# Optimization experiments

Hardware: AMD Instinct MI355X
Metric: run time of the kernel (lower is better)

Reference implementation:

```python
import jax, jax.numpy as jnp
import numpy as np

EPS_NORM = 1e-10
EPS_EXP = 1e-6


def setup_inputs() -> dict:
    key = jax.random.key(0)
    k1, k2 = jax.random.split(key)
    B, F, H, W = 16, 2048, 8, 8
    X = jax.random.normal(k1, (B, F, H, W), dtype=jnp.float32)
    M = jax.random.normal(k2, (B, F, H, W), dtype=jnp.float32)
    return {"X": X, "M": M}


def reference(X, M):
    B, F, H, W = X.shape
    N = H * W
    X = X.reshape(B, F, N)
    M = M.reshape(B, F, N)

    # feature centering over dim=-2 (the feature axis of (B, F, N))
    X = X - X.mean(axis=1, keepdims=True)
    M = M - M.mean(axis=1, keepdims=True)

    # feature_normalize: L2 norm over dim 1, keepdim, + eps
    X = X / (jnp.linalg.norm(X, axis=1, keepdims=True) + EPS_NORM)
    M = M / (jnp.linalg.norm(M, axis=1, keepdims=True) + EPS_NORM)

    # MatmulTopkLoss: S = X @ M^T over spatial N -> (B, F, F)
    S = jnp.einsum('bfn,bgn->bfg', X, M)
    YX = S + jnp.transpose(S, (0, 2, 1))  # symmetrize
    P = jax.nn.softmax(YX, axis=-1)

    k = F // 2
    value, idx = jax.lax.top_k(P, k)  # (B, F, k) values desc, indices
    value_sum = value.sum(axis=-1, keepdims=True)
    row_pos = jnp.arange(F)[None, :, None]  # (1, F, 1)
    dist = jnp.abs(idx - row_pos).astype(value.dtype)
    C_xy = (value * dist / value_sum).mean(axis=-1)  # (B, F)

    xy = jnp.exp(-C_xy + C_xy.min() - EPS_EXP)
    return jnp.reshape(xy.mean(), (1,))
```

## Files before the change

kernel.cpp:

```cpp
#include <hip/hip_runtime.h>
#include <hip/hip_bf16.h>
#include <math.h>

#define B_   16
#define F_   2048
#define N_   64
#define K_   1024
#define YP   2056

typedef short bf16x8 __attribute__((ext_vector_type(8)));
typedef float v4f    __attribute__((ext_vector_type(4)));

__device__ __forceinline__ float wave_sum(float v) {
#pragma unroll
  for (int off = 32; off > 0; off >>= 1) v += __shfl_down(v, off, 64);
  return v;
}
__device__ __forceinline__ float wave_max(float v) {
#pragma unroll
  for (int off = 32; off > 0; off >>= 1) v = fmaxf(v, __shfl_down(v, off, 64));
  return v;
}

__device__ __forceinline__ unsigned f2bf(float x) {
  const unsigned u = __float_as_uint(x);
  return (u + 0x7FFFu + ((u >> 16) & 1u)) >> 16;
}
__device__ __forceinline__ float bf2f(unsigned us) {
  return __uint_as_float(us << 16);
}
__device__ __forceinline__ unsigned ord2u16(unsigned T) {
  return (T & 0x8000u) ? (T ^ 0x8000u) : (T ^ 0xFFFFu);
}
__device__ __forceinline__ unsigned ordpair(unsigned wd) {
  return wd ^ (0x80008000u | (((wd & 0x80008000u) >> 15) * 0x7FFFu));
}

__global__ __launch_bounds__(256) void stats_kernel(
    const float* __restrict__ X, const float* __restrict__ M,
    float* __restrict__ P) {
  __shared__ float red[4][N_][4];
  const int tid = threadIdx.x;
  const int b = blockIdx.x >> 4;
  const int fb = blockIdx.x & 15;
  const int f0 = fb * 128;
  const int fi = tid >> 6, n = tid & 63;
  float sx = 0.f, sxx = 0.f, sm = 0.f, smm = 0.f;
#pragma unroll 4
  for (int j = 0; j < 32; ++j) {
    const int f = f0 + fi + 4 * j;
    const size_t gi = ((size_t)b * F_ + f) * N_ + n;
    const float x = X[gi];
    const float m = M[gi];
    sx += x; sxx += x * x; sm += m; smm += m * m;
  }
  red[fi][n][0] = sx; red[fi][n][1] = sxx;
  red[fi][n][2] = sm; red[fi][n][3] = smm;
  __syncthreads();
  const int wn = tid & 63, word = tid >> 6;
  const float s = red[0][wn][word] + red[1][wn][word] +
                  red[2][wn][word] + red[3][wn][word];
  P[(((size_t)b * N_ + wn) * 4 + word) * 16 + fb] = s;
}

__global__ __launch_bounds__(256) void normbf_kernel(
    const float* __restrict__ X, const float* __restrict__ M,
    const float* __restrict__ P,
    short* __restrict__ Xb16, short* __restrict__ Mb16) {
  const int tid = threadIdx.x;
  const int b = blockIdx.x >> 4;
  const int f0 = (blockIdx.x & 15) * 128;
  const int n = tid & 63;
  const float* base = P + (((size_t)b * N_ + n) * 4) * 16;
  float acc4[4];
#pragma unroll
  for (int wj = 0; wj < 4; ++wj) {
    float s = 0.f;
#pragma unroll
    for (int i = 0; i < 16; ++i) s += base[16 * wj + i];
    acc4[wj] = s;
  }
  const float sx = acc4[0], sxx = acc4[1], sm = acc4[2], smm = acc4[3];
  const float mux = sx * (1.f / F_), mum = sm * (1.f / F_);
  const float rx = 1.f / (sqrtf(fmaxf(sxx - (float)F_ * mux * mux, 0.f)) + 1e-10f);
  const float rm = 1.f / (sqrtf(fmaxf(smm - (float)F_ * mum * mum, 0.f)) + 1e-10f);
  const int s_ = n >> 5, q_ = (n >> 3) & 3, j_ = n & 7;
#pragma unroll 4
  for (int jj = 0; jj < 32; ++jj) {
    const int f = f0 + (tid >> 6) + 4 * jj;
    const size_t gi = ((size_t)b * F_ + f) * N_ + n;
    const int t16 = f >> 4, nl = f & 15;
    const size_t pi = (((size_t)b * 128 + t16) * 2 + s_) * 512 +
                      (q_ * 16 + nl) * 8 + j_;
    Xb16[pi] = (short)f2bf((X[gi] - mux) * rx);
    Mb16[pi] = (short)f2bf((M[gi] - mum) * rm);
  }
}

__global__ __launch_bounds__(512)
__attribute__((amdgpu_waves_per_eu(4, 4)))
void rows_kernel(
    const short* __restrict__ Xb16, const short* __restrict__ Mb16,
    float* __restrict__ C) {
  __shared__ unsigned short yxu[16 * YP];
  __shared__ unsigned histS[8 * 256];

  const int tid = threadIdx.x;
  const int w = tid >> 6, lane = tid & 63;
  const int nl = lane & 15, q = lane >> 4;
  const int b = blockIdx.x >> 7;
  const int f0 = (blockIdx.x & 127) * 16;
  const int g0 = 256 * w;

  const short* __restrict__ Xb = Xb16 + (size_t)b * F_ * N_;
  const short* __restrict__ Mb = Mb16 + (size_t)b * F_ * N_;

  const short* Axp = Xb + (size_t)(f0 >> 4) * 1024 + lane * 8;
  const short* Amp = Mb + (size_t)(f0 >> 4) * 1024 + lane * 8;
  const bf16x8 ax0 = *(const bf16x8*)(Axp);
  const bf16x8 ax1 = *(const bf16x8*)(Axp + 512);
  const bf16x8 am0 = *(const bf16x8*)(Amp);
  const bf16x8 am1 = *(const bf16x8*)(Amp + 512);

  v4f acc[16];
#pragma unroll
  for (int t = 0; t < 16; ++t) acc[t] = (v4f)(0.f);

#pragma unroll
  for (int t = 0; t < 16; ++t) {
    const short* Bmp = Mb + (size_t)(16 * w + t) * 1024 + lane * 8;
    const short* Bxp = Xb + (size_t)(16 * w + t) * 1024 + lane * 8;
    const bf16x8 bm0 = *(const bf16x8*)(Bmp);
    const bf16x8 bm1 = *(const bf16x8*)(Bmp + 512);
    const bf16x8 bx0 = *(const bf16x8*)(Bxp);
    const bf16x8 bx1 = *(const bf16x8*)(Bxp + 512);
    acc[t] = __builtin_amdgcn_mfma_f32_16x16x32_bf16(ax0, bm0, acc[t], 0, 0, 0);
    acc[t] = __builtin_amdgcn_mfma_f32_16x16x32_bf16(ax1, bm1, acc[t], 0, 0, 0);
    acc[t] = __builtin_amdgcn_mfma_f32_16x16x32_bf16(am0, bx0, acc[t], 0, 0, 0);
    acc[t] = __builtin_amdgcn_mfma_f32_16x16x32_bf16(am1, bx1, acc[t], 0, 0, 0);
  }

#pragma unroll
  for (int t = 0; t < 16; ++t) {
    const int col = g0 + 16 * t + nl;
#pragma unroll
    for (int r = 0; r < 4; ++r)
      yxu[(4 * q + r) * YP + col] = (unsigned short)f2bf(acc[t][r]);
  }
  __syncthreads();

  unsigned* wh = &histS[w << 8];
#pragma unroll 1
  for (int r4 = 0; r4 < 2; ++r4) {
    const int row = 2 * w + r4;
    const int frow = f0 + row;
    const uint4* rp = (const uint4*)(yxu + row * YP);

    unsigned pk[16];
    unsigned kmin = 0xFFFFFFFFu, kmax = 0u;
#pragma unroll
    for (int j = 0; j < 4; ++j) {
      const uint4 tt = rp[lane + 64 * j];
      const unsigned wds[4] = {tt.x, tt.y, tt.z, tt.w};
#pragma unroll
      for (int c = 0; c < 4; ++c) {
        const unsigned o = ordpair(wds[c]);
        pk[4 * j + c] = o;
        const unsigned o0 = o & 0xFFFFu, o1 = o >> 16;
        kmin = min(kmin, min(o0, o1));
        kmax = max(kmax, max(o0, o1));
      }
    }
#pragma unroll
    for (int off = 32; off > 0; off >>= 1) {
      kmin = min(kmin, (unsigned)__shfl_down((int)kmin, off, 64));
      kmax = max(kmax, (unsigned)__shfl_down((int)kmax, off, 64));
    }
    kmin = (unsigned)__shfl((int)kmin, 0, 64);
    kmax = (unsigned)__shfl((int)kmax, 0, 64);

    unsigned lo = kmin, R = kmax - kmin, krem = K_;
    unsigned T, tie_need;
    if (R == 0) {
      T = lo; tie_need = krem;
    } else {
      for (;;) {
        const int pos = 31 - __builtin_clz(R);
        const int sh = (pos > 7) ? (pos - 7) : 0;
#pragma unroll
        for (int i = 0; i < 4; ++i) wh[lane + 64 * i] = 0u;
        __builtin_amdgcn_wave_barrier();
#pragma unroll
        for (int c = 0; c < 16; ++c) {
          const unsigned o = pk[c];
          const unsigned d0 = (o & 0xFFFFu) - lo;
          const unsigned d1 = (o >> 16) - lo;
          if (d0 <= R) atomicAdd(&wh[d0 >> sh], 1u);
          if (d1 <= R) atomicAdd(&wh[d1 >> sh], 1u);
        }
        __builtin_amdgcn_wave_barrier();
        unsigned h[4];
#pragma unroll
        for (int i = 0; i < 4; ++i) h[i] = wh[4 * lane + i];
        unsigned s3 = h[3], s2 = h[2] + s3, s1 = h[1] + s2, s0 = h[0] + s1;
        unsigned tot = s0;
#pragma unroll
        for (int off = 1; off < 64; off <<= 1) {
          const unsigned v = __shfl_down(tot, off, 64);
          if (lane + off < 64) tot += v;
        }
        const unsigned above = tot - s0;
        const unsigned S[4] = {above + s0, above + s1, above + s2, above + s3};
        unsigned packed = 0;
        bool found = false;
#pragma unroll
        for (int i = 0; i < 4; ++i) {
          const unsigned Sip1 = S[i] - h[i];
          if (S[i] >= krem && Sip1 < krem) {
            packed = ((unsigned)(4 * lane + i) << 16) | Sip1;
            found = true;
          }
        }
        const unsigned long long bm = __ballot(found);
        const int winner = __ffsll(bm) - 1;
        packed = (unsigned)__shfl((int)packed, winner, 64);
        const unsigned D = packed >> 16;
        krem -= (packed & 0xFFFFu);
        if (sh == 0) { T = lo + D; tie_need = krem; break; }
        lo += (D << sh);
        R = (1u << sh) - 1u;
      }
    }

    float vs = 0.f, ws = 0.f;
    unsigned cnt[4];
#pragma unroll
    for (int j = 0; j < 4; ++j) {
      cnt[j] = 0;
#pragma unroll
      for (int c = 0; c < 4; ++c) {
        const unsigned o = pk[4 * j + c];
        const unsigned oo[2] = {o & 0xFFFFu, o >> 16};
#pragma unroll
        for (int i = 0; i < 2; ++i) {
          const int g = 512 * j + 8 * lane + 2 * c + i;
          if (oo[i] > T) {
            const float pv = __expf(bf2f(ord2u16(oo[i])));
            vs += pv; ws += pv * fabsf((float)(g - frow));
          } else if (oo[i] == T) cnt[j]++;
        }
      }
    }
    const float ptie = __expf(bf2f(ord2u16(T)));

    unsigned pA = cnt[0] | (cnt[1] << 16), pB = cnt[2] | (cnt[3] << 16);
    unsigned iA = pA, iB = pB;
#pragma unroll
    for (int off = 1; off < 64; off <<= 1) {
      const unsigned vA = __shfl_up(iA, off, 64);
      const unsigned vB = __shfl_up(iB, off, 64);
      if (lane >= off) { iA += vA; iB += vB; }
    }
    const unsigned eA = iA - pA, eB = iB - pB;
    const unsigned tA = (unsigned)__shfl((int)iA, 63, 64);
    const unsigned tB = (unsigned)__shfl((int)iB, 63, 64);
    unsigned G[4];
    G[0] = 0;
    G[1] = G[0] + (tA & 0xFFFFu);
    G[2] = G[1] + (tA >> 16);
    G[3] = G[2] + (tB & 0xFFFFu);
#pragma unroll
    for (int j = 0; j < 4; ++j) {
      if (cnt[j]) {
        const unsigned off = (j < 2) ? ((eA >> (16 * j)) & 0xFFFFu)
                                     : ((eB >> (16 * (j - 2))) & 0xFFFFu);
        unsigned cc = 0;
#pragma unroll
        for (int c = 0; c < 4; ++c) {
          const unsigned o = pk[4 * j + c];
          const unsigned oo[2] = {o & 0xFFFFu, o >> 16};
#pragma unroll
          for (int i = 0; i < 2; ++i) {
            if (oo[i] == T) {
              if (G[j] + off + cc < tie_need) {
                const int g = 512 * j + 8 * lane + 2 * c + i;
                vs += ptie; ws += ptie * fabsf((float)(g - frow));
              }
              cc++;
            }
          }
        }
      }
    }

    vs = wave_sum(vs); ws = wave_sum(ws);
    if (lane == 0)
      C[(size_t)b * F_ + frow] = (ws / vs) * (1.f / (float)K_);
  }
}

__global__ __launch_bounds__(1024) void final_kernel(
    const float* __restrict__ C, unsigned* __restrict__ out) {
  __shared__ float red[16];
  const int tid = threadIdx.x;
  const int wave = tid >> 6, lane = tid & 63;
  float v[32];
  float mn = 3.4e38f;
#pragma unroll
  for (int i = 0; i < 32; ++i) {
    v[i] = C[tid + 1024 * i];
    mn = fminf(mn, v[i]);
  }
  mn = -wave_max(-mn);
  if (lane == 0) red[wave] = mn;
  __syncthreads();
  float cmin = red[0];
  for (int w = 1; w < 16; ++w) cmin = fminf(cmin, red[w]);
  __syncthreads();
  float s = 0.f;
#pragma unroll
  for (int i = 0; i < 32; ++i) s += expf(cmin - v[i] - 1e-6f);
  s = wave_sum(s);
  if (lane == 0) red[wave] = s;
  __syncthreads();
  if (tid == 0) {
    float tot = 0.f;
    for (int w = 0; w < 16; ++w) tot += red[w];
    const float res = tot * (1.f / 32768.f);
    const __hip_bfloat16 hb = __float2bfloat16(res);
    const unsigned short u = *(const unsigned short*)&hb;
    out[0] = ((unsigned)u << 16) | (unsigned)u;
  }
}

extern "C" void kernel_launch(void* const* d_in, const int* in_sizes, int n_in,
                              void* d_out, int out_size, void* d_ws, size_t ws_size,
                              hipStream_t stream) {
  const float* X = (const float*)d_in[0];
  const float* M = (const float*)d_in[1];
  short* Xb16 = (short*)d_ws;
  short* Mb16 = Xb16 + (size_t)B_ * F_ * N_;
  float* C = (float*)(Mb16 + (size_t)B_ * F_ * N_);
  float* P = C + (size_t)B_ * F_;

  stats_kernel<<<dim3(B_ * 16), dim3(256), 0, stream>>>(X, M, P);
  normbf_kernel<<<dim3(B_ * 16), dim3(256), 0, stream>>>(X, M, P, Xb16, Mb16);
  rows_kernel<<<dim3(B_ * (F_ / 16)), dim3(512), 0, stream>>>(Xb16, Mb16, C);
  final_kernel<<<dim3(1), dim3(1024), 0, stream>>>(C, (unsigned*)d_out);
}
```

Measured before the change: 201.0 us.

## Split stats and normalize into more blocks with separate partial-sum reduction kernel

The stats and normalize kernels now launch four times as many blocks (1024 instead of 256), each covering 32 features, so the mostly memory-bound preprocessing can use more CUs. Partial sums move to a feature-block-major layout, and a new small reduce kernel combines them once. Normalize then reads a single float4 per column instead of re-summing 64 partials in every block. This adds one more kernel launch and an extra round trip through global memory in exchange.

```diff
diff --git a/kernel.cpp b/kernel.cpp
--- a/kernel.cpp
+++ b/kernel.cpp
@@ -41,13 +41,13 @@
     float* __restrict__ P) {
   __shared__ float red[4][N_][4];
   const int tid = threadIdx.x;
-  const int b = blockIdx.x >> 4;
-  const int fb = blockIdx.x & 15;
-  const int f0 = fb * 128;
+  const int b = blockIdx.x >> 6;
+  const int fb = blockIdx.x & 63;
+  const int f0 = fb * 32;
   const int fi = tid >> 6, n = tid & 63;
   float sx = 0.f, sxx = 0.f, sm = 0.f, smm = 0.f;
-#pragma unroll 4
-  for (int j = 0; j < 32; ++j) {
+#pragma unroll
+  for (int j = 0; j < 8; ++j) {
     const int f = f0 + fi + 4 * j;
     const size_t gi = ((size_t)b * F_ + f) * N_ + n;
     const float x = X[gi];
@@ -60,33 +60,39 @@
   const int wn = tid & 63, word = tid >> 6;
   const float s = red[0][wn][word] + red[1][wn][word] +
                   red[2][wn][word] + red[3][wn][word];
-  P[(((size_t)b * N_ + wn) * 4 + word) * 16 + fb] = s;
+  P[(size_t)fb * 4096 + b * 256 + wn * 4 + word] = s;
+}
+
+__global__ __launch_bounds__(256) void reduce_kernel(
+    const float* __restrict__ P, float* __restrict__ S) {
+  const int i = blockIdx.x * 256 + threadIdx.x;
+  float s0 = 0.f, s1 = 0.f, s2 = 0.f, s3 = 0.f;
+#pragma unroll
+  for (int fb = 0; fb < 64; fb += 4) {
+    s0 += P[(size_t)fb * 4096 + i];
+    s1 += P[(size_t)(fb + 1) * 4096 + i];
+    s2 += P[(size_t)(fb + 2) * 4096 + i];
+    s3 += P[(size_t)(fb + 3) * 4096 + i];
+  }
+  S[i] = (s0 + s1) + (s2 + s3);
 }
 
 __global__ __launch_bounds__(256) void normbf_kernel(
     const float* __restrict__ X, const float* __restrict__ M,
-    const float* __restrict__ P,
+    const float* __restrict__ S,
     short* __restrict__ Xb16, short* __restrict__ Mb16) {
   const int tid = threadIdx.x;
-  const int b = blockIdx.x >> 4;
-  const int f0 = (blockIdx.x & 15) * 128;
+  const int b = blockIdx.x >> 6;
+  const int f0 = (blockIdx.x & 63) * 32;
   const int n = tid & 63;
-  const float* base = P + (((size_t)b * N_ + n) * 4) * 16;
-  float acc4[4];
-#pragma unroll
-  for (int wj = 0; wj < 4; ++wj) {
-    float s = 0.f;
-#pragma unroll
-    for (int i = 0; i < 16; ++i) s += base[16 * wj + i];
-    acc4[wj] = s;
-  }
-  const float sx = acc4[0], sxx = acc4[1], sm = acc4[2], smm = acc4[3];
+  const float4 s4 = ((const float4*)S)[b * 64 + n];
+  const float sx = s4.x, sxx = s4.y, sm = s4.z, smm = s4.w;
   const float mux = sx * (1.f / F_), mum = sm * (1.f / F_);
   const float rx = 1.f / (sqrtf(fmaxf(sxx - (float)F_ * mux * mux, 0.f)) + 1e-10f);
   const float rm = 1.f / (sqrtf(fmaxf(smm - (float)F_ * mum * mum, 0.f)) + 1e-10f);
   const int s_ = n >> 5, q_ = (n >> 3) & 3, j_ = n & 7;
-#pragma unroll 4
-  for (int jj = 0; jj < 32; ++jj) {
+#pragma unroll
+  for (int jj = 0; jj < 8; ++jj) {
     const int f = f0 + (tid >> 6) + 4 * jj;
     const size_t gi = ((size_t)b * F_ + f) * N_ + n;
     const int t16 = f >> 4, nl = f & 15;
@@ -342,9 +348,11 @@
   short* Mb16 = Xb16 + (size_t)B_ * F_ * N_;
   float* C = (float*)(Mb16 + (size_t)B_ * F_ * N_);
   float* P = C + (size_t)B_ * F_;
-
-  stats_kernel<<<dim3(B_ * 16), dim3(256), 0, stream>>>(X, M, P);
-  normbf_kernel<<<dim3(B_ * 16), dim3(256), 0, stream>>>(X, M, P, Xb16, Mb16);
+  float* S = P + (size_t)64 * 4096;
+
+  stats_kernel<<<dim3(B_ * 64), dim3(256), 0, stream>>>(X, M, P);
+  reduce_kernel<<<dim3(16), dim3(256), 0, stream>>>(P, S);
+  normbf_kernel<<<dim3(B_ * 64), dim3(256), 0, stream>>>(X, M, S, Xb16, Mb16);
   rows_kernel<<<dim3(B_ * (F_ / 16)), dim3(512), 0, stream>>>(Xb16, Mb16, C);
   final_kernel<<<dim3(1), dim3(1024), 0, stream>>>(C, (unsigned*)d_out);
 }
```

Result: no change. 199.5 us (-0.7%).
